# Performance work log

Hardware: AMD Instinct MI355X
Metric: run time of the kernel (lower is better)

## Reference

```python
import jax, jax.numpy as jnp
import numpy as np
import math

B, S, H, E, TOPK, NHEADS = 8, 512, 1024, 8, 2, 8
CAP = int(B * S * 1.5 * TOPK / E)  # 1536


def _linear(x, w, b):
    # torch nn.Linear convention: y = x @ w.T + b, w: [out, in]
    return x @ w.T + b


def _mha(x, in_w, in_b, out_w, out_b, n_heads):
    # torch nn.MultiheadAttention self-attention, eval mode (no dropout)
    Bx, Sx, D = x.shape
    dh = D // n_heads
    qkv = x @ in_w.T + in_b                      # [B,S,3D]
    q, k, v = jnp.split(qkv, 3, axis=-1)
    def heads(t):
        return t.reshape(Bx, Sx, n_heads, dh).transpose(0, 2, 1, 3)  # [B,h,S,dh]
    q, k, v = heads(q), heads(k), heads(v)
    scores = jnp.einsum('bhqd,bhkd->bhqk', q, k) / math.sqrt(dh)
    attn = jax.nn.softmax(scores, axis=-1)
    o = jnp.einsum('bhqk,bhkd->bhqd', attn, v)   # [B,h,S,dh]
    o = o.transpose(0, 2, 1, 3).reshape(Bx, Sx, D)
    return o @ out_w.T + out_b


def setup_inputs() -> dict:
    key = jax.random.key(0)
    ks = jax.random.split(key, 24)
    sc = 0.02
    d = {
        'hidden_states': jax.random.normal(ks[0], (B, S, H), jnp.float32),
        'pos_emb': jax.random.normal(ks[1], (S, H), jnp.float32) * sc,
        'se_w1': jax.random.normal(ks[2], (H // 4, 1), jnp.float32) * sc,
        'se_b1': jnp.zeros((H // 4,), jnp.float32),
        'se_w2': jax.random.normal(ks[3], (H // 4, H // 4), jnp.float32) * sc,
        'se_b2': jnp.zeros((H // 4,), jnp.float32),
        'sexp_w': jax.random.normal(ks[4], (H, H // 4), jnp.float32) * sc,
        'sexp_b': jnp.zeros((H,), jnp.float32),
        'te_w1': jax.random.normal(ks[5], (H, H + 2), jnp.float32) * sc,
        'te_b1': jnp.zeros((H,), jnp.float32),
        'te_w2': jax.random.normal(ks[6], (H, H), jnp.float32) * sc,
        'te_b2': jnp.zeros((H,), jnp.float32),
        'attn_in_w': jax.random.normal(ks[7], (3 * H, H), jnp.float32) * sc,
        'attn_in_b': jnp.zeros((3 * H,), jnp.float32),
        'attn_out_w': jax.random.normal(ks[8], (H, H), jnp.float32) * sc,
        'attn_out_b': jnp.zeros((H,), jnp.float32),
        'tr_w1': jax.random.normal(ks[9], (H, H), jnp.float32) * sc,
        'tr_b1': jnp.zeros((H,), jnp.float32),
        'tr_w2': jax.random.normal(ks[10], (E, H), jnp.float32) * sc,
        'tr_b2': jnp.zeros((E,), jnp.float32),
    }
    return d


def reference(hidden_states, pos_emb, se_w1, se_b1, se_w2, se_b2, sexp_w, sexp_b,
              te_w1, te_b1, te_w2, te_b2, attn_in_w, attn_in_b, attn_out_w, attn_out_b,
              tr_w1, tr_b1, tr_w2, tr_b2):
    b, s, h = hidden_states.shape
    timestamps = jnp.arange(s, dtype=hidden_states.dtype)           # [S]
    seasonality = jnp.sin(timestamps * 2 * jnp.pi / 24)             # [S]
    ts_b = jnp.broadcast_to(timestamps, (b, s))
    se_b = jnp.broadcast_to(seasonality, (b, s))

    position_embeddings = pos_emb[:s][None]                          # [1,S,H]
    seas = jax.nn.relu(_linear(se_b[..., None], se_w1, se_b1))       # [B,S,H/4]
    seas = _linear(seas, se_w2, se_b2)
    seasonal_embeddings = _linear(seas, sexp_w, sexp_b)              # [B,S,H]

    time_features = jnp.stack([ts_b, se_b], axis=-1)                 # [B,S,2]
    combined = jnp.concatenate([hidden_states, time_features], -1)   # [B,S,H+2]
    enc = jax.nn.relu(_linear(combined, te_w1, te_b1))
    enc = _linear(enc, te_w2, te_b2)
    enc = enc + position_embeddings + seasonal_embeddings
    enc = _mha(enc, attn_in_w, attn_in_b, attn_out_w, attn_out_b, NHEADS)

    logits = _linear(jax.nn.relu(_linear(enc, tr_w1, tr_b1)), tr_w2, tr_b2)  # [B,S,E]
    router_probs = jax.nn.softmax(logits, axis=-1)
    top_k_probs, top_k_idx = jax.lax.top_k(router_probs, TOPK)
    top_k_probs = top_k_probs / top_k_probs.sum(-1, keepdims=True)

    capacity = int(b * s * 1.5 * TOPK / E)
    # top-k indices are distinct per token, so summed one-hots replicate the
    # python loop's slot-0 writes exactly.
    onehot = jax.nn.one_hot(top_k_idx, E, dtype=router_probs.dtype)  # [B,S,K,E]
    disp0 = onehot.sum(axis=2)                                        # [B,S,E]
    comb0 = jnp.einsum('bske,bsk->bse', onehot, top_k_probs)          # [B,S,E]
    dispatch = jnp.zeros((b, s, E, capacity), router_probs.dtype).at[:, :, :, 0].set(disp0)
    combine = jnp.zeros((b, s, E, capacity), router_probs.dtype).at[:, :, :, 0].set(comb0)

    p_mean = router_probs.mean(axis=(0, 1))
    aux_loss = jnp.sum(p_mean * jnp.log(p_mean * E + 1e-9))
    return dispatch, combine, router_probs, aux_loss
```

## Files before the change

### kernel.cpp

```cpp
#include <hip/hip_runtime.h>
#include <hip/hip_bf16.h>


#define Hh 1024

typedef __attribute__((ext_vector_type(8))) short short8v;
typedef __attribute__((ext_vector_type(4))) float f32x4;

static __device__ __forceinline__ ushort f2bf(float x) {
  uint u = __float_as_uint(x);
  u += 0x7FFF + ((u >> 16) & 1);
  return (ushort)(u >> 16);
}
static __device__ __forceinline__ float bf2f(ushort h) {
  return __uint_as_float(((uint)h) << 16);
}

template<int EPI, bool RELU, bool HAS_BN, bool HAS_BSN>
__global__ __launch_bounds__(256, 2) void mgemm_k(
    const ushort* __restrict__ A, int lda, long long sAmaj, long long sAmin, int aHi, int aLo,
    const ushort* __restrict__ Bf, int BNT, int BKC, long long sBmaj, long long sBmin,
    float* __restrict__ Cf, ushort* __restrict__ Ch, int ldc, long long sCmaj, long long sCmin,
    int splitOff,
    ushort* __restrict__ pK, ushort* __restrict__ pV,
    int Kd, int zdiv,
    const float* __restrict__ bN, const float* __restrict__ bSN, int ldbs, int smod,
    float alpha)
{
  int gx = gridDim.x, gy = gridDim.y;
  int lin = (blockIdx.z * gy + blockIdx.y) * gx + blockIdx.x;
  int nwg = gx * gy * gridDim.z;
  int cpx = nwg >> 3;
  int swz = (lin & 7) * cpx + (lin >> 3);
  int bz = swz / (gx * gy);
  int rem = swz - bz * (gx * gy);
  int by = rem / gx, bx = rem - by * gx;

  int zj = bz / zdiv, zi = bz - zj * zdiv;
  A += (size_t)zj * sAmaj + (size_t)zi * sAmin;
  const ushort* bfb = Bf + (size_t)zj * sBmaj + (size_t)zi * sBmin;
  long long coff = (long long)zj * sCmaj + (long long)zi * sCmin;

  int m0 = by * 128, n0 = bx * 128;

  __shared__ __align__(16) ushort smem[16384];

  int t = threadIdx.x;
  int l = t & 63, w = t >> 6;
  int wm = w >> 1, wn = w & 1;

  f32x4 acc[4][4];
#pragma unroll
  for (int i = 0; i < 4; ++i)
#pragma unroll
    for (int j = 0; j < 4; ++j) acc[i][j] = (f32x4){0.f, 0.f, 0.f, 0.f};

  int srow = t >> 1;
  int sc = (t & 1) * 2;
  const ushort* gAh = A + (size_t)(m0 + srow) * lda + aHi + sc * 8;
  const ushort* gAl = A + (size_t)(m0 + srow) * lda + aLo + sc * 8;
  int wsw = ((srow >> 1) & 7) << 4;
  int wo0 = (srow * 64 + sc * 16) ^ wsw;
  int wo1 = wo0 ^ 16;

  int aoff[4];
#pragma unroll
  for (int mi = 0; mi < 4; ++mi) {
    int row = wm * 64 + mi * 16 + (l & 15);
    aoff[mi] = (row * 64 + (l >> 4) * 16) ^ (((row >> 1) & 7) << 4);
  }

  const ushort* bph[4];
  const ushort* bpl[4];
  int ntg0 = (n0 >> 4) + wn * 4;
#pragma unroll
  for (int ni = 0; ni < 4; ++ni) {
    bph[ni] = bfb + ((size_t)(ntg0 + ni) * BKC) * 512 + l * 8;
    bpl[ni] = bfb + ((size_t)(BNT + ntg0 + ni) * BKC) * 512 + l * 8;
  }

  int4 a0h0, a0h1, a0l0, a0l1, a1h0, a1h1, a1l0, a1l1;
  short8v B0h[4], B0l[4], B1h[4], B1l[4];

#define LOADA0(s) { a0h0 = *(const int4*)(gAh + (s)*32); a0h1 = *(const int4*)(gAh + (s)*32 + 8); \
                    a0l0 = *(const int4*)(gAl + (s)*32); a0l1 = *(const int4*)(gAl + (s)*32 + 8); }
#define LOADA1(s) { a1h0 = *(const int4*)(gAh + (s)*32); a1h1 = *(const int4*)(gAh + (s)*32 + 8); \
                    a1l0 = *(const int4*)(gAl + (s)*32); a1l1 = *(const int4*)(gAl + (s)*32 + 8); }
#define STOREA(h0, h1, l0, l1, base) { char* nb = (char*)smem + (base); \
    *(int4*)(nb + wo0) = h0; *(int4*)(nb + wo1) = h1; \
    *(int4*)(nb + 8192 + wo0) = l0; *(int4*)(nb + 8192 + wo1) = l1; }
#define LOADB(BH, BL, s) { _Pragma("unroll") \
    for (int ni = 0; ni < 4; ++ni) { \
      BH[ni] = *(const short8v*)(bph[ni] + (size_t)(s) * 512); \
      BL[ni] = *(const short8v*)(bpl[ni] + (size_t)(s) * 512); } }
#define MFMA_STEP(ahb, alb, BH, BL) { \
    short8v ah[4], al[4]; \
    _Pragma("unroll") for (int mi = 0; mi < 4; ++mi) \
      ah[mi] = *(const short8v*)((char*)smem + (ahb) + aoff[mi]); \
    _Pragma("unroll") for (int mi = 0; mi < 4; ++mi) \
      al[mi] = *(const short8v*)((char*)smem + (alb) + aoff[mi]); \
    _Pragma("unroll") for (int ni = 0; ni < 4; ++ni) \
      _Pragma("unroll") for (int mi = 0; mi < 4; ++mi) \
        acc[mi][ni] = __builtin_amdgcn_mfma_f32_16x16x32_bf16(ah[mi], BH[ni], acc[mi][ni], 0, 0, 0); \
    _Pragma("unroll") for (int ni = 0; ni < 4; ++ni) \
      _Pragma("unroll") for (int mi = 0; mi < 4; ++mi) \
        acc[mi][ni] = __builtin_amdgcn_mfma_f32_16x16x32_bf16(al[mi], BH[ni], acc[mi][ni], 0, 0, 0); \
    _Pragma("unroll") for (int ni = 0; ni < 4; ++ni) \
      _Pragma("unroll") for (int mi = 0; mi < 4; ++mi) \
        acc[mi][ni] = __builtin_amdgcn_mfma_f32_16x16x32_bf16(ah[mi], BL[ni], acc[mi][ni], 0, 0, 0); }

  int nt = Kd >> 5;
  LOADA0(0); LOADB(B0h, B0l, 0);
  LOADA1(1); LOADB(B1h, B1l, 1);
  STOREA(a0h0, a0h1, a0l0, a0l1, 0);
  __syncthreads();
  for (int s2 = 0; s2 < nt; s2 += 2) {
    if (s2 + 2 < nt) LOADA0(s2 + 2);
    MFMA_STEP(0, 8192, B0h, B0l);
    if (s2 + 2 < nt) LOADB(B0h, B0l, s2 + 2);
    STOREA(a1h0, a1h1, a1l0, a1l1, 16384);
    __syncthreads();
    if (s2 + 3 < nt) LOADA1(s2 + 3);
    MFMA_STEP(16384, 24576, B1h, B1l);
    if (s2 + 3 < nt) LOADB(B1h, B1l, s2 + 3);
    if (s2 + 2 < nt) STOREA(a0h0, a0h1, a0l0, a0l1, 0);
    __syncthreads();
  }
#undef LOADA0
#undef LOADA1
#undef STOREA
#undef LOADB
#undef MFMA_STEP

#pragma unroll
  for (int mi = 0; mi < 4; ++mi)
#pragma unroll
    for (int j = 0; j < 4; ++j) {
      int m = m0 + wm * 64 + mi * 16 + (l >> 4) * 4 + j;
#pragma unroll
      for (int ni = 0; ni < 4; ++ni) {
        int n = n0 + wn * 64 + ni * 16 + (l & 15);
        float x = acc[mi][ni][j] * alpha;
        if (HAS_BN) x += bN[n];
        if (HAS_BSN) x += bSN[(size_t)(m % smod) * ldbs + n];
        if (RELU) x = fmaxf(x, 0.f);
        acc[mi][ni][j] = x;
      }
    }

  if (EPI == 0) {
    float* Fs = (float*)smem;
#pragma unroll
    for (int p = 0; p < 2; ++p) {
      __syncthreads();
      if (wm == p) {
#pragma unroll
        for (int mi = 0; mi < 4; ++mi)
#pragma unroll
          for (int j = 0; j < 4; ++j) {
            int r = mi * 16 + (l >> 4) * 4 + j;
#pragma unroll
            for (int ni = 0; ni < 4; ++ni) {
              int c = wn * 64 + ni * 16 + (l & 15);
              *(float*)((char*)Fs + ((r * 512 + c * 4) ^ ((r & 7) << 4))) = acc[mi][ni][j];
            }
          }
      }
      __syncthreads();
#pragma unroll
      for (int r8 = 0; r8 < 8; ++r8) {
        int idx = r8 * 256 + t;
        int row = idx >> 5, slot = idx & 31;
        int4 v = *(const int4*)((char*)Fs + ((row * 512 + slot * 16) ^ ((row & 7) << 4)));
        *(int4*)(Cf + coff + (size_t)(m0 + p * 64 + row) * ldc + n0 + slot * 4) = v;
      }
    }
  } else {
    __syncthreads();
    ushort* Es = smem;
    bool isQ = (EPI == 1) || (n0 < 1024);
    bool isK = (EPI == 2) && !isQ && (n0 < 2048);
    int bb = m0 >> 9, s0 = m0 & 511;
    int hh2 = isK ? ((n0 - 1024) >> 7) : ((n0 - 2048) >> 7);
    size_t kvb = (size_t)(bb * 8 + hh2) * 131072;
#pragma unroll
    for (int pass = 0; pass < 2; ++pass) {
      if (isQ) {
#pragma unroll
        for (int mi = 0; mi < 4; ++mi)
#pragma unroll
          for (int j = 0; j < 4; ++j) {
            int lr = wm * 64 + mi * 16 + (l >> 4) * 4 + j;
#pragma unroll
            for (int ni = 0; ni < 4; ++ni) {
              int lcb = (wn * 64 + ni * 16 + (l & 15)) * 2;
              float x = acc[mi][ni][j];
              ushort h = f2bf(x);
              ushort vv = (pass == 0) ? h : f2bf(x - bf2f(h));
              *(ushort*)((char*)Es + ((lr * 256 + lcb) ^ ((lr & 7) << 4))) = vv;
            }
          }
      } else if (isK) {
#pragma unroll
        for (int mi = 0; mi < 4; ++mi)
#pragma unroll
          for (int j = 0; j < 4; ++j) {
            int lr = wm * 64 + mi * 16 + (l >> 4) * 4 + j;
#pragma unroll
            for (int ni = 0; ni < 4; ++ni) {
              int lcb = (wn * 64 + ni * 16 + (l & 15)) * 2;
              float x = acc[mi][ni][j];
              ushort h = f2bf(x);
              ushort vv = (pass == 0) ? h : f2bf(x - bf2f(h));
              *(ushort*)((char*)Es + ((lr * 256 + lcb) ^ ((lr & 7) << 4))) = vv;
            }
          }
      } else {
#pragma unroll
        for (int mi = 0; mi < 4; ++mi)
#pragma unroll
          for (int j = 0; j < 4; ++j) {
            int cc = (wm * 64 + mi * 16 + (l >> 4) * 4 + j) * 2;
#pragma unroll
            for (int ni = 0; ni < 4; ++ni) {
              int rr = wn * 64 + ni * 16 + (l & 15);
              float x = acc[mi][ni][j];
              ushort h = f2bf(x);
              ushort vv = (pass == 0) ? h : f2bf(x - bf2f(h));
              *(ushort*)((char*)Es + ((rr * 256 + cc) ^ ((rr & 7) << 4))) = vv;
            }
          }
      }
      __syncthreads();
      if (isQ) {
        int off = (pass == 0) ? 0 : splitOff;
#pragma unroll
        for (int r = 0; r < 8; ++r) {
          int idx = r * 256 + t;
          int row = idx >> 4, cb = (idx & 15) * 16;
          int4 v = *(const int4*)((char*)Es + ((row * 256 + cb) ^ ((row & 7) << 4)));
          *(int4*)((char*)(Ch + coff + (size_t)(m0 + row) * ldc + off + n0) + cb) = v;
        }
      } else if (isK) {
#pragma unroll
        for (int sw = 0; sw < 8; ++sw) {
          int idx = sw * 256 + t;
          int f = idx >> 6, l2 = idx & 63;
          int st = f >> 2, dc = f & 3;
          int row = st * 16 + (l2 & 15);
          int colB = (dc * 32 + ((l2 >> 4) << 3)) * 2;
          short8v v = *(const short8v*)((char*)Es + ((row * 256 + colB) ^ ((row & 7) << 4)));
          *(short8v*)(pK + kvb + (size_t)((pass * 32 + (s0 >> 4) + st) * 4 + dc) * 512 + l2 * 8) = v;
        }
      } else {
#pragma unroll
        for (int sw = 0; sw < 8; ++sw) {
          int idx = sw * 256 + t;
          int f = idx >> 6, l2 = idx & 63;
          int dt = f >> 2, sch = f & 3;
          int row = dt * 16 + (l2 & 15);
          int colB = (sch * 32 + ((l2 >> 4) << 3)) * 2;
          short8v v = *(const short8v*)((char*)Es + ((row * 256 + colB) ^ ((row & 7) << 4)));
          *(short8v*)(pV + kvb + (size_t)((pass * 8 + dt) * 16 + (s0 >> 5) + sch) * 512 + l2 * 8) = v;
        }
      }
      if (pass == 0) __syncthreads();
    }
  }
}

__global__ __launch_bounds__(64) void convertf_k(
    const float* __restrict__ W, int ldw, ushort* __restrict__ Wf, int NT, int KC)
{
  int kc = blockIdx.x, nt2 = blockIdx.y, l = threadIdx.x;
  const float* src = W + (size_t)(nt2 * 16 + (l & 15)) * ldw + kc * 32 + ((l >> 4) << 3);
  ushort h8[8], l8[8];
#pragma unroll
  for (int j = 0; j < 8; ++j) {
    float x = src[j];
    h8[j] = f2bf(x);
    l8[j] = f2bf(x - bf2f(h8[j]));
  }
  *(int4*)(Wf + ((size_t)nt2 * KC + kc) * 512 + l * 8) = *(int4*)h8;
  *(int4*)(Wf + ((size_t)(NT + nt2) * KC + kc) * 512 + l * 8) = *(int4*)l8;
}

__global__ __launch_bounds__(256) void convert_k(
    const float* __restrict__ W, int lda, ushort* __restrict__ Whl, int K)
{
  int r = blockIdx.x;
  int c = threadIdx.x * 4;
  const float* src = W + (size_t)r * lda + c;
  float x0 = src[0], x1 = src[1], x2 = src[2], x3 = src[3];
  ushort4 h, lo;
  h.x = f2bf(x0); lo.x = f2bf(x0 - bf2f(h.x));
  h.y = f2bf(x1); lo.y = f2bf(x1 - bf2f(h.y));
  h.z = f2bf(x2); lo.z = f2bf(x2 - bf2f(h.z));
  h.w = f2bf(x3); lo.w = f2bf(x3 - bf2f(h.w));
  ushort* dst = Whl + (size_t)r * 2 * K;
  *(ushort4*)&dst[c] = h;
  *(ushort4*)&dst[K + c] = lo;
}

__global__ __launch_bounds__(256) void precompute_k(
    const float* __restrict__ pos_emb,
    const float* __restrict__ se_w1, const float* __restrict__ se_b1,
    const float* __restrict__ se_w2, const float* __restrict__ se_b2,
    const float* __restrict__ sexp_w, const float* __restrict__ sexp_b,
    const float* __restrict__ te_w1, const float* __restrict__ te_b1,
    float* __restrict__ psea, float* __restrict__ bias1)
{
  int s = blockIdx.x, t = threadIdx.x;
  float ts = (float)s;
  float se = sinf(((ts * 2.0f) * 3.14159274101257324f) / 24.0f);
  __shared__ float l1[256], l2[256];
  l1[t] = fmaxf(se * se_w1[t] + se_b1[t], 0.f);
  __syncthreads();
  {
    float a = se_b2[t];
    const float* wr = se_w2 + (size_t)t * 256;
    for (int i = 0; i < 256; ++i) a += l1[i] * wr[i];
    l2[t] = a;
  }
  __syncthreads();
#pragma unroll
  for (int r = 0; r < 4; ++r) {
    int h = r * 256 + t;
    float v = sexp_b[h];
    const float* wr = sexp_w + (size_t)h * 256;
    for (int j = 0; j < 256; ++j) v += l2[j] * wr[j];
    psea[s * Hh + h] = pos_emb[s * Hh + h] + v;
    bias1[s * Hh + h] = te_b1[h] + ts * te_w1[(size_t)h * 1026 + 1024]
                                 + se * te_w1[(size_t)h * 1026 + 1025];
  }
}

__global__ __launch_bounds__(256) void softmax2_k(float* __restrict__ S)
{
  int row = blockIdx.x * 4 + (threadIdx.x >> 6);
  int lane = threadIdx.x & 63;
  float* p = S + (size_t)row * 512;
  float4 a = *(float4*)&p[lane * 4];
  float4 b = *(float4*)&p[256 + lane * 4];
  float m = fmaxf(fmaxf(fmaxf(a.x, a.y), fmaxf(a.z, a.w)),
                  fmaxf(fmaxf(b.x, b.y), fmaxf(b.z, b.w)));
#pragma unroll
  for (int off = 32; off; off >>= 1) m = fmaxf(m, __shfl_xor(m, off));
  a.x = expf(a.x - m); a.y = expf(a.y - m); a.z = expf(a.z - m); a.w = expf(a.w - m);
  b.x = expf(b.x - m); b.y = expf(b.y - m); b.z = expf(b.z - m); b.w = expf(b.w - m);
  float s = a.x + a.y + a.z + a.w + b.x + b.y + b.z + b.w;
#pragma unroll
  for (int off = 32; off; off >>= 1) s += __shfl_xor(s, off);
  float inv = 1.f / s;
  a.x *= inv; a.y *= inv; a.z *= inv; a.w *= inv;
  b.x *= inv; b.y *= inv; b.z *= inv; b.w *= inv;
  ushort* u = (ushort*)S + (size_t)row * 1024;
  ushort4 ha, la, hb, lb;
  ha.x = f2bf(a.x); la.x = f2bf(a.x - bf2f(ha.x));
  ha.y = f2bf(a.y); la.y = f2bf(a.y - bf2f(ha.y));
  ha.z = f2bf(a.z); la.z = f2bf(a.z - bf2f(ha.z));
  ha.w = f2bf(a.w); la.w = f2bf(a.w - bf2f(ha.w));
  hb.x = f2bf(b.x); lb.x = f2bf(b.x - bf2f(hb.x));
  hb.y = f2bf(b.y); lb.y = f2bf(b.y - bf2f(hb.y));
  hb.z = f2bf(b.z); lb.z = f2bf(b.z - bf2f(hb.z));
  hb.w = f2bf(b.w); lb.w = f2bf(b.w - bf2f(hb.w));
  *(ushort4*)&u[lane * 4] = ha;
  *(ushort4*)&u[512 + lane * 4] = la;
  *(ushort4*)&u[256 + lane * 4] = hb;
  *(ushort4*)&u[768 + lane * 4] = lb;
}

__global__ __launch_bounds__(256) void tr2_k(
    const float* __restrict__ h1, const float* __restrict__ w,
    const float* __restrict__ bias, float* __restrict__ logits)
{
  int wid = threadIdx.x >> 6, lane = threadIdx.x & 63;
  int t = blockIdx.x * 4 + wid;
  const float* x = h1 + (size_t)t * Hh;
  float acc[8];
#pragma unroll
  for (int e = 0; e < 8; ++e) acc[e] = 0.f;
  for (int k = lane; k < Hh; k += 64) {
    float xv = x[k];
#pragma unroll
    for (int e = 0; e < 8; ++e) acc[e] += xv * w[e * Hh + k];
  }
#pragma unroll
  for (int e = 0; e < 8; ++e) {
#pragma unroll
    for (int off = 32; off; off >>= 1) acc[e] += __shfl_xor(acc[e], off);
  }
  if (lane == 0) {
#pragma unroll
    for (int e = 0; e < 8; ++e) logits[(size_t)t * 8 + e] = acc[e] + bias[e];
  }
}

__global__ __launch_bounds__(256) void fill0_k(float4* __restrict__ p, long long n4)
{
  long long i = (long long)blockIdx.x * 256 + threadIdx.x;
  long long stride = (long long)gridDim.x * 256;
  float4 z = make_float4(0.f, 0.f, 0.f, 0.f);
  for (; i < n4; i += stride) p[i] = z;
}

__global__ __launch_bounds__(256) void router_k(
    float* __restrict__ out, float* __restrict__ partials)
{
  int t = blockIdx.x * 256 + threadIdx.x;
  float* lg = out + 100663296 + (size_t)t * 8;
  float p[8];
#pragma unroll
  for (int e = 0; e < 8; ++e) p[e] = lg[e];
  float m = p[0];
#pragma unroll
  for (int e = 1; e < 8; ++e) m = fmaxf(m, p[e]);
  float s = 0.f;
#pragma unroll
  for (int e = 0; e < 8; ++e) { p[e] = expf(p[e] - m); s += p[e]; }
  float inv = 1.f / s;
#pragma unroll
  for (int e = 0; e < 8; ++e) p[e] *= inv;
#pragma unroll
  for (int e = 0; e < 8; ++e) lg[e] = p[e];

  int i0 = 0; float v0 = p[0];
#pragma unroll
  for (int e = 1; e < 8; ++e) if (p[e] > v0) { v0 = p[e]; i0 = e; }
  int i1 = -1; float v1 = -1.f;
#pragma unroll
  for (int e = 0; e < 8; ++e) if (e != i0 && p[e] > v1) { v1 = p[e]; i1 = e; }
  float wn = 1.f / (v0 + v1);
  size_t db = (size_t)t * (8 * 1536);
  out[db + (size_t)i0 * 1536] = 1.f;
  out[db + (size_t)i1 * 1536] = 1.f;
  out[50331648 + db + (size_t)i0 * 1536] = v0 * wn;
  out[50331648 + db + (size_t)i1 * 1536] = v1 * wn;

  __shared__ float red[256];
#pragma unroll
  for (int e = 0; e < 8; ++e) {
    red[threadIdx.x] = p[e];
    __syncthreads();
    for (int st = 128; st; st >>= 1) {
      if (threadIdx.x < st) red[threadIdx.x] += red[threadIdx.x + st];
      __syncthreads();
    }
    if (threadIdx.x == 0) partials[blockIdx.x * 8 + e] = red[0];
    __syncthreads();
  }
}

__global__ __launch_bounds__(64) void aux_k(float* __restrict__ partials,
                                            float* __restrict__ out)
{
  int lane = threadIdx.x;
  float v = 0.f;
  if (lane < 8) {
    float s = 0.f;
    for (int b = 0; b < 16; ++b) s += partials[b * 8 + lane];
    float pm = s / 4096.f;
    v = pm * logf(pm * 8.f + 1e-9f);
  }
#pragma unroll
  for (int off = 4; off; off >>= 1) v += __shfl_xor(v, off);
  if (lane == 0) out[100696064] = v;
  partials[lane] = 0.f;
  partials[64 + lane] = 0.f;
}

extern "C" void kernel_launch(void* const* d_in, const int* in_sizes, int n_in,
                              void* d_out, int out_size, void* d_ws, size_t ws_size,
                              hipStream_t stream)
{
  const float* hidden = (const float*)d_in[0];
  const float* pos_emb = (const float*)d_in[1];
  const float* se_w1 = (const float*)d_in[2];
  const float* se_b1 = (const float*)d_in[3];
  const float* se_w2 = (const float*)d_in[4];
  const float* se_b2 = (const float*)d_in[5];
  const float* sexp_w = (const float*)d_in[6];
  const float* sexp_b = (const float*)d_in[7];
  const float* te_w1 = (const float*)d_in[8];
  const float* te_b1 = (const float*)d_in[9];
  const float* te_w2 = (const float*)d_in[10];
  const float* te_b2 = (const float*)d_in[11];
  const float* ain_w = (const float*)d_in[12];
  const float* ain_b = (const float*)d_in[13];
  const float* aout_w = (const float*)d_in[14];
  const float* aout_b = (const float*)d_in[15];
  const float* tr_w1 = (const float*)d_in[16];
  const float* tr_b1 = (const float*)d_in[17];
  const float* tr_w2 = (const float*)d_in[18];
  const float* tr_b2 = (const float*)d_in[19];
  float* out = (float*)d_out;

  char* arena = (char*)d_out;
  ushort* W1f  = (ushort*)(arena + 0);
  ushort* W2f  = (ushort*)(arena + 4194304);
  ushort* Waf  = (ushort*)(arena + 8388608);
  ushort* Wof  = (ushort*)(arena + 20971520);
  ushort* Wtf  = (ushort*)(arena + 25165824);
  ushort* hid2 = (ushort*)(arena + 29360128);
  ushort* enc1 = (ushort*)(arena + 46137344);
  ushort* enc2 = (ushort*)(arena + 62914560);
  ushort* qbuf = (ushort*)(arena + 79691776);
  ushort* Kf   = (ushort*)(arena + 96468992);
  ushort* Vf   = (ushort*)(arena + 113246208);
  float*  scor = (float*)(arena + 130023424);
  ushort* attno= (ushort*)(arena + 197132288);
  ushort* encf = (ushort*)(arena + 213909504);
  float*  h1   = (float*)(arena + 230686720);
  float*  psea = (float*)(arena + 247463936);
  float*  bias1= (float*)(arena + 249561088);
  float*  parts= out + 51380224;
  float*  lgts = out + 100663296;

  convertf_k<<<dim3(32, 64), 64, 0, stream>>>(te_w1, 1026, W1f, 64, 32);
  convertf_k<<<dim3(32, 64), 64, 0, stream>>>(te_w2, 1024, W2f, 64, 32);
  convertf_k<<<dim3(32, 192), 64, 0, stream>>>(ain_w, 1024, Waf, 192, 32);
  convertf_k<<<dim3(32, 64), 64, 0, stream>>>(aout_w, 1024, Wof, 64, 32);
  convertf_k<<<dim3(32, 64), 64, 0, stream>>>(tr_w1, 1024, Wtf, 64, 32);
  convert_k<<<4096, 256, 0, stream>>>(hidden, 1024, hid2, 1024);

  precompute_k<<<512, 256, 0, stream>>>(pos_emb, se_w1, se_b1, se_w2, se_b2,
                                        sexp_w, sexp_b, te_w1, te_b1, psea, bias1);

  mgemm_k<1, true, false, true><<<dim3(8, 32, 1), 256, 0, stream>>>(
      hid2, 2048, 0, 0, 0, 1024,
      W1f, 64, 32, 0, 0,
      nullptr, enc1, 2048, 0, 0, 1024, nullptr, nullptr,
      1024, 1, nullptr, bias1, 1024, 512, 1.f);

  mgemm_k<1, false, true, true><<<dim3(8, 32, 1), 256, 0, stream>>>(
      enc1, 2048, 0, 0, 0, 1024,
      W2f, 64, 32, 0, 0,
      nullptr, enc2, 2048, 0, 0, 1024, nullptr, nullptr,
      1024, 1, te_b2, psea, 1024, 512, 1.f);

  mgemm_k<2, false, true, false><<<dim3(24, 32, 1), 256, 0, stream>>>(
      enc2, 2048, 0, 0, 0, 1024,
      Waf, 192, 32, 0, 0,
      nullptr, qbuf, 2048, 0, 0, 1024, Kf, Vf,
      1024, 1, ain_b, nullptr, 1, 1, 1.f);

  mgemm_k<0, false, false, false><<<dim3(4, 4, 64), 256, 0, stream>>>(
      qbuf, 2048, 1048576, 128, 0, 1024,
      Kf, 32, 4, 1048576, 131072,
      scor, nullptr, 512, 2097152, 262144, 0, nullptr, nullptr,
      128, 8, nullptr, nullptr, 1, 1, 0.08838834764831845f);

  softmax2_k<<<8192, 256, 0, stream>>>(scor);

  mgemm_k<1, false, false, false><<<dim3(1, 4, 64), 256, 0, stream>>>(
      (const ushort*)scor, 1024, 4194304, 524288, 0, 512,
      Vf, 8, 16, 1048576, 131072,
      nullptr, attno, 2048, 1048576, 128, 1024, nullptr, nullptr,
      512, 8, nullptr, nullptr, 1, 1, 1.f);

  mgemm_k<1, false, true, false><<<dim3(8, 32, 1), 256, 0, stream>>>(
      attno, 2048, 0, 0, 0, 1024,
      Wof, 64, 32, 0, 0,
      nullptr, encf, 2048, 0, 0, 1024, nullptr, nullptr,
      1024, 1, aout_b, nullptr, 1, 1, 1.f);

  mgemm_k<0, true, true, false><<<dim3(8, 32, 1), 256, 0, stream>>>(
      encf, 2048, 0, 0, 0, 1024,
      Wtf, 64, 32, 0, 0,
      h1, nullptr, 1024, 0, 0, 0, nullptr, nullptr,
      1024, 1, tr_b1, nullptr, 1, 1, 1.f);

  tr2_k<<<1024, 256, 0, stream>>>(h1, tr_w2, tr_b2, lgts);

  fill0_k<<<4096, 256, 0, stream>>>((float4*)out, 25165824LL);

  router_k<<<16, 256, 0, stream>>>(out, parts);
  aux_k<<<1, 64, 0, stream>>>(parts, out);
}
```

Measured before the change: 481.4 us.

## Fuse QK^T, softmax and PV into a single attention kernel

Replaces the three-kernel attention path (score GEMM writing fp32 scores, a separate softmax pass, and a PV GEMM reading split-bf16 probabilities) with one fused kernel. Each 512-thread block keeps a 128x512 score tile in registers, reduces row max and sum through shared memory, and feeds split-bf16 probabilities through LDS into the PV MFMAs. This removes the large score-buffer round trip through global memory and two launches. The five weight-conversion launches are also merged into one, and the Q/K epilogue branches are deduplicated. The cost is very high register pressure from the 128-float score accumulator per thread plus an extra occupancy constraint.

```diff
diff --git a/kernel.cpp b/kernel.cpp
--- a/kernel.cpp
+++ b/kernel.cpp
@@ -185,22 +185,7 @@
     size_t kvb = (size_t)(bb * 8 + hh2) * 131072;
 #pragma unroll
     for (int pass = 0; pass < 2; ++pass) {
-      if (isQ) {
-#pragma unroll
-        for (int mi = 0; mi < 4; ++mi)
-#pragma unroll
-          for (int j = 0; j < 4; ++j) {
-            int lr = wm * 64 + mi * 16 + (l >> 4) * 4 + j;
-#pragma unroll
-            for (int ni = 0; ni < 4; ++ni) {
-              int lcb = (wn * 64 + ni * 16 + (l & 15)) * 2;
-              float x = acc[mi][ni][j];
-              ushort h = f2bf(x);
-              ushort vv = (pass == 0) ? h : f2bf(x - bf2f(h));
-              *(ushort*)((char*)Es + ((lr * 256 + lcb) ^ ((lr & 7) << 4))) = vv;
-            }
-          }
-      } else if (isK) {
+      if (!(EPI == 2 && !isQ && !isK)) {
 #pragma unroll
         for (int mi = 0; mi < 4; ++mi)
 #pragma unroll
@@ -269,10 +254,265 @@
   }
 }
 
-__global__ __launch_bounds__(64) void convertf_k(
-    const float* __restrict__ W, int ldw, ushort* __restrict__ Wf, int NT, int KC)
-{
-  int kc = blockIdx.x, nt2 = blockIdx.y, l = threadIdx.x;
+__global__ __launch_bounds__(512, 2) void attn_k(
+    const ushort* __restrict__ qbuf, const ushort* __restrict__ Kf,
+    const ushort* __restrict__ Vf, ushort* __restrict__ attno)
+{
+  int qt = blockIdx.x;
+  int bh = blockIdx.y;
+  int b = bh >> 3, h = bh & 7;
+
+  __shared__ __align__(16) ushort smem[32768];
+  __shared__ float rowred[1024];
+
+  int t = threadIdx.x;
+  int l = t & 63, w = t >> 6;
+  int wm = w >> 2, wn = w & 3;
+
+  {
+    int srow = t >> 2, sc = t & 3;
+    const ushort* gQ = qbuf + (size_t)(b * 512 + qt * 128 + srow) * 2048 + h * 128 + sc * 8;
+    int wo = (srow * 64 + sc * 16) ^ (((srow >> 1) & 7) << 4);
+#pragma unroll
+    for (int ks = 0; ks < 4; ++ks) {
+      int4 vh = *(const int4*)(gQ + ks * 32);
+      int4 vl = *(const int4*)(gQ + 1024 + ks * 32);
+      *(int4*)((char*)smem + ks * 8192 + wo) = vh;
+      *(int4*)((char*)smem + 32768 + ks * 8192 + wo) = vl;
+    }
+  }
+
+  int aoff[4];
+#pragma unroll
+  for (int mi = 0; mi < 4; ++mi) {
+    int row = wm * 64 + mi * 16 + (l & 15);
+    aoff[mi] = (row * 64 + (l >> 4) * 16) ^ (((row >> 1) & 7) << 4);
+  }
+
+  __syncthreads();
+
+  f32x4 S[4][4][2];
+#pragma unroll
+  for (int c = 0; c < 4; ++c)
+#pragma unroll
+    for (int mi = 0; mi < 4; ++mi)
+#pragma unroll
+      for (int ni = 0; ni < 2; ++ni) S[c][mi][ni] = (f32x4){0.f, 0.f, 0.f, 0.f};
+
+  const ushort* Kb = Kf + (size_t)bh * 131072 + l * 8;
+#pragma unroll
+  for (int c = 0; c < 4; ++c) {
+#pragma unroll
+    for (int ks = 0; ks < 4; ++ks) {
+      short8v bhf[2], blf[2], ahf[4], alf[4];
+#pragma unroll
+      for (int ni = 0; ni < 2; ++ni) {
+        int ntk = c * 8 + wn * 2 + ni;
+        bhf[ni] = *(const short8v*)(Kb + (size_t)(ntk * 4 + ks) * 512);
+        blf[ni] = *(const short8v*)(Kb + (size_t)((32 + ntk) * 4 + ks) * 512);
+      }
+#pragma unroll
+      for (int mi = 0; mi < 4; ++mi) {
+        ahf[mi] = *(const short8v*)((char*)smem + ks * 8192 + aoff[mi]);
+        alf[mi] = *(const short8v*)((char*)smem + 32768 + ks * 8192 + aoff[mi]);
+      }
+#pragma unroll
+      for (int ni = 0; ni < 2; ++ni)
+#pragma unroll
+        for (int mi = 0; mi < 4; ++mi)
+          S[c][mi][ni] = __builtin_amdgcn_mfma_f32_16x16x32_bf16(ahf[mi], bhf[ni], S[c][mi][ni], 0, 0, 0);
+#pragma unroll
+      for (int ni = 0; ni < 2; ++ni)
+#pragma unroll
+        for (int mi = 0; mi < 4; ++mi)
+          S[c][mi][ni] = __builtin_amdgcn_mfma_f32_16x16x32_bf16(alf[mi], bhf[ni], S[c][mi][ni], 0, 0, 0);
+#pragma unroll
+      for (int ni = 0; ni < 2; ++ni)
+#pragma unroll
+        for (int mi = 0; mi < 4; ++mi)
+          S[c][mi][ni] = __builtin_amdgcn_mfma_f32_16x16x32_bf16(ahf[mi], blf[ni], S[c][mi][ni], 0, 0, 0);
+    }
+  }
+
+  const float scale = 0.08838834764831845f;
+  float inv16[4][4];
+  {
+    float mx[4][4];
+#pragma unroll
+    for (int mi = 0; mi < 4; ++mi)
+#pragma unroll
+      for (int j = 0; j < 4; ++j) {
+        float m2 = -3.0e38f;
+#pragma unroll
+        for (int c = 0; c < 4; ++c)
+#pragma unroll
+          for (int ni = 0; ni < 2; ++ni) m2 = fmaxf(m2, S[c][mi][ni][j]);
+#pragma unroll
+        for (int off = 8; off; off >>= 1) m2 = fmaxf(m2, __shfl_xor(m2, off));
+        mx[mi][j] = m2;
+      }
+    if ((l & 15) == 0) {
+#pragma unroll
+      for (int mi = 0; mi < 4; ++mi)
+#pragma unroll
+        for (int j = 0; j < 4; ++j) {
+          int row = wm * 64 + mi * 16 + (l >> 4) * 4 + j;
+          rowred[wn * 128 + row] = mx[mi][j];
+        }
+    }
+    __syncthreads();
+#pragma unroll
+    for (int mi = 0; mi < 4; ++mi)
+#pragma unroll
+      for (int j = 0; j < 4; ++j) {
+        int row = wm * 64 + mi * 16 + (l >> 4) * 4 + j;
+        float m2 = fmaxf(fmaxf(rowred[row], rowred[128 + row]),
+                         fmaxf(rowred[256 + row], rowred[384 + row]));
+        mx[mi][j] = m2 * scale;
+      }
+    float sm[4][4];
+#pragma unroll
+    for (int mi = 0; mi < 4; ++mi)
+#pragma unroll
+      for (int j = 0; j < 4; ++j) {
+        float s2 = 0.f;
+#pragma unroll
+        for (int c = 0; c < 4; ++c)
+#pragma unroll
+          for (int ni = 0; ni < 2; ++ni) {
+            float p = __expf(fmaf(S[c][mi][ni][j], scale, -mx[mi][j]));
+            S[c][mi][ni][j] = p;
+            s2 += p;
+          }
+#pragma unroll
+        for (int off = 8; off; off >>= 1) s2 += __shfl_xor(s2, off);
+        sm[mi][j] = s2;
+      }
+    if ((l & 15) == 0) {
+#pragma unroll
+      for (int mi = 0; mi < 4; ++mi)
+#pragma unroll
+        for (int j = 0; j < 4; ++j) {
+          int row = wm * 64 + mi * 16 + (l >> 4) * 4 + j;
+          rowred[512 + wn * 128 + row] = sm[mi][j];
+        }
+    }
+    __syncthreads();
+#pragma unroll
+    for (int mi = 0; mi < 4; ++mi)
+#pragma unroll
+      for (int j = 0; j < 4; ++j) {
+        int row = wm * 64 + mi * 16 + (l >> 4) * 4 + j;
+        float s2 = rowred[512 + row] + rowred[640 + row]
+                 + rowred[768 + row] + rowred[896 + row];
+        inv16[mi][j] = 1.f / s2;
+      }
+  }
+
+  f32x4 O[4][2];
+#pragma unroll
+  for (int mi = 0; mi < 4; ++mi)
+#pragma unroll
+    for (int ni = 0; ni < 2; ++ni) O[mi][ni] = (f32x4){0.f, 0.f, 0.f, 0.f};
+
+  const ushort* Vb = Vf + (size_t)bh * 131072 + l * 8;
+#pragma unroll
+  for (int c = 0; c < 4; ++c) {
+    __syncthreads();
+#pragma unroll
+    for (int mi = 0; mi < 4; ++mi)
+#pragma unroll
+      for (int j = 0; j < 4; ++j) {
+        int row = wm * 64 + mi * 16 + (l >> 4) * 4 + j;
+        int sw2 = ((row >> 1) & 7) << 4;
+#pragma unroll
+        for (int ni = 0; ni < 2; ++ni) {
+          float p = S[c][mi][ni][j] * inv16[mi][j];
+          ushort hh = f2bf(p);
+          ushort ll2 = f2bf(p - bf2f(hh));
+          int off = (row * 64 + (ni * 16 + (l & 15)) * 2) ^ sw2;
+          *(ushort*)((char*)smem + wn * 8192 + off) = hh;
+          *(ushort*)((char*)smem + 32768 + wn * 8192 + off) = ll2;
+        }
+      }
+    __syncthreads();
+#pragma unroll
+    for (int ks = 0; ks < 4; ++ks) {
+      short8v pah[4], pal[4], vbh[2], vbl[2];
+#pragma unroll
+      for (int ni = 0; ni < 2; ++ni) {
+        int ntd = wn * 2 + ni;
+        vbh[ni] = *(const short8v*)(Vb + (size_t)(ntd * 16 + c * 4 + ks) * 512);
+        vbl[ni] = *(const short8v*)(Vb + (size_t)((8 + ntd) * 16 + c * 4 + ks) * 512);
+      }
+#pragma unroll
+      for (int mi = 0; mi < 4; ++mi) {
+        pah[mi] = *(const short8v*)((char*)smem + ks * 8192 + aoff[mi]);
+        pal[mi] = *(const short8v*)((char*)smem + 32768 + ks * 8192 + aoff[mi]);
+      }
+#pragma unroll
+      for (int ni = 0; ni < 2; ++ni)
+#pragma unroll
+        for (int mi = 0; mi < 4; ++mi)
+          O[mi][ni] = __builtin_amdgcn_mfma_f32_16x16x32_bf16(pah[mi], vbh[ni], O[mi][ni], 0, 0, 0);
+#pragma unroll
+      for (int ni = 0; ni < 2; ++ni)
+#pragma unroll
+        for (int mi = 0; mi < 4; ++mi)
+          O[mi][ni] = __builtin_amdgcn_mfma_f32_16x16x32_bf16(pal[mi], vbh[ni], O[mi][ni], 0, 0, 0);
+#pragma unroll
+      for (int ni = 0; ni < 2; ++ni)
+#pragma unroll
+        for (int mi = 0; mi < 4; ++mi)
+          O[mi][ni] = __builtin_amdgcn_mfma_f32_16x16x32_bf16(pah[mi], vbl[ni], O[mi][ni], 0, 0, 0);
+    }
+  }
+
+  __syncthreads();
+  ushort* Es = smem;
+  size_t coff = (size_t)b * 1048576 + (size_t)h * 128;
+  int m0 = qt * 128;
+#pragma unroll
+  for (int pass = 0; pass < 2; ++pass) {
+#pragma unroll
+    for (int mi = 0; mi < 4; ++mi)
+#pragma unroll
+      for (int j = 0; j < 4; ++j) {
+        int lr = wm * 64 + mi * 16 + (l >> 4) * 4 + j;
+#pragma unroll
+        for (int ni = 0; ni < 2; ++ni) {
+          int lcb = (wn * 32 + ni * 16 + (l & 15)) * 2;
+          float x = O[mi][ni][j];
+          ushort hh = f2bf(x);
+          ushort vv = (pass == 0) ? hh : f2bf(x - bf2f(hh));
+          *(ushort*)((char*)Es + ((lr * 256 + lcb) ^ ((lr & 7) << 4))) = vv;
+        }
+      }
+    __syncthreads();
+    int off = (pass == 0) ? 0 : 1024;
+#pragma unroll
+    for (int r = 0; r < 4; ++r) {
+      int idx = r * 512 + t;
+      int row = idx >> 4, cb = (idx & 15) * 16;
+      int4 v = *(const int4*)((char*)Es + ((row * 256 + cb) ^ ((row & 7) << 4)));
+      *(int4*)((char*)(attno + coff + (size_t)(m0 + row) * 2048 + off) + cb) = v;
+    }
+    if (pass == 0) __syncthreads();
+  }
+}
+
+__global__ __launch_bounds__(64) void convall_k(
+    const float* __restrict__ te_w1, const float* __restrict__ te_w2,
+    const float* __restrict__ ain_w, const float* __restrict__ aout_w,
+    const float* __restrict__ tr_w1, ushort* __restrict__ base)
+{
+  int kc = blockIdx.x, y = blockIdx.y, l = threadIdx.x;
+  const float* W; int ldw, NT, nt2; ushort* dst;
+  if (y < 64)       { W = te_w1;  ldw = 1026; NT = 64;  nt2 = y;       dst = base; }
+  else if (y < 128) { W = te_w2;  ldw = 1024; NT = 64;  nt2 = y - 64;  dst = base + 2097152; }
+  else if (y < 320) { W = ain_w;  ldw = 1024; NT = 192; nt2 = y - 128; dst = base + 4194304; }
+  else if (y < 384) { W = aout_w; ldw = 1024; NT = 64;  nt2 = y - 320; dst = base + 10485760; }
+  else              { W = tr_w1;  ldw = 1024; NT = 64;  nt2 = y - 384; dst = base + 12582912; }
   const float* src = W + (size_t)(nt2 * 16 + (l & 15)) * ldw + kc * 32 + ((l >> 4) << 3);
   ushort h8[8], l8[8];
 #pragma unroll
@@ -281,8 +521,8 @@
     h8[j] = f2bf(x);
     l8[j] = f2bf(x - bf2f(h8[j]));
   }
-  *(int4*)(Wf + ((size_t)nt2 * KC + kc) * 512 + l * 8) = *(int4*)h8;
-  *(int4*)(Wf + ((size_t)(NT + nt2) * KC + kc) * 512 + l * 8) = *(int4*)l8;
+  *(int4*)(dst + ((size_t)nt2 * 32 + kc) * 512 + l * 8) = *(int4*)h8;
+  *(int4*)(dst + ((size_t)(NT + nt2) * 32 + kc) * 512 + l * 8) = *(int4*)l8;
 }
 
 __global__ __launch_bounds__(256) void convert_k(
@@ -333,41 +573,6 @@
     bias1[s * Hh + h] = te_b1[h] + ts * te_w1[(size_t)h * 1026 + 1024]
                                  + se * te_w1[(size_t)h * 1026 + 1025];
   }
-}
-
-__global__ __launch_bounds__(256) void softmax2_k(float* __restrict__ S)
-{
-  int row = blockIdx.x * 4 + (threadIdx.x >> 6);
-  int lane = threadIdx.x & 63;
-  float* p = S + (size_t)row * 512;
-  float4 a = *(float4*)&p[lane * 4];
-  float4 b = *(float4*)&p[256 + lane * 4];
-  float m = fmaxf(fmaxf(fmaxf(a.x, a.y), fmaxf(a.z, a.w)),
-                  fmaxf(fmaxf(b.x, b.y), fmaxf(b.z, b.w)));
-#pragma unroll
-  for (int off = 32; off; off >>= 1) m = fmaxf(m, __shfl_xor(m, off));
-  a.x = expf(a.x - m); a.y = expf(a.y - m); a.z = expf(a.z - m); a.w = expf(a.w - m);
-  b.x = expf(b.x - m); b.y = expf(b.y - m); b.z = expf(b.z - m); b.w = expf(b.w - m);
-  float s = a.x + a.y + a.z + a.w + b.x + b.y + b.z + b.w;
-#pragma unroll
-  for (int off = 32; off; off >>= 1) s += __shfl_xor(s, off);
-  float inv = 1.f / s;
-  a.x *= inv; a.y *= inv; a.z *= inv; a.w *= inv;
-  b.x *= inv; b.y *= inv; b.z *= inv; b.w *= inv;
-  ushort* u = (ushort*)S + (size_t)row * 1024;
-  ushort4 ha, la, hb, lb;
-  ha.x = f2bf(a.x); la.x = f2bf(a.x - bf2f(ha.x));
-  ha.y = f2bf(a.y); la.y = f2bf(a.y - bf2f(ha.y));
-  ha.z = f2bf(a.z); la.z = f2bf(a.z - bf2f(ha.z));
-  ha.w = f2bf(a.w); la.w = f2bf(a.w - bf2f(ha.w));
-  hb.x = f2bf(b.x); lb.x = f2bf(b.x - bf2f(hb.x));
-  hb.y = f2bf(b.y); lb.y = f2bf(b.y - bf2f(hb.y));
-  hb.z = f2bf(b.z); lb.z = f2bf(b.z - bf2f(hb.z));
-  hb.w = f2bf(b.w); lb.w = f2bf(b.w - bf2f(hb.w));
-  *(ushort4*)&u[lane * 4] = ha;
-  *(ushort4*)&u[512 + lane * 4] = la;
-  *(ushort4*)&u[256 + lane * 4] = hb;
-  *(ushort4*)&u[768 + lane * 4] = lb;
 }
 
 __global__ __launch_bounds__(256) void tr2_k(
@@ -496,18 +701,13 @@
   float* out = (float*)d_out;
 
   char* arena = (char*)d_out;
-  ushort* W1f  = (ushort*)(arena + 0);
-  ushort* W2f  = (ushort*)(arena + 4194304);
-  ushort* Waf  = (ushort*)(arena + 8388608);
-  ushort* Wof  = (ushort*)(arena + 20971520);
-  ushort* Wtf  = (ushort*)(arena + 25165824);
+  ushort* Wbase= (ushort*)(arena + 0);
   ushort* hid2 = (ushort*)(arena + 29360128);
   ushort* enc1 = (ushort*)(arena + 46137344);
   ushort* enc2 = (ushort*)(arena + 62914560);
   ushort* qbuf = (ushort*)(arena + 79691776);
   ushort* Kf   = (ushort*)(arena + 96468992);
   ushort* Vf   = (ushort*)(arena + 113246208);
-  float*  scor = (float*)(arena + 130023424);
   ushort* attno= (ushort*)(arena + 197132288);
   ushort* encf = (ushort*)(arena + 213909504);
   float*  h1   = (float*)(arena + 230686720);
@@ -516,57 +716,40 @@
   float*  parts= out + 51380224;
   float*  lgts = out + 100663296;
 
-  convertf_k<<<dim3(32, 64), 64, 0, stream>>>(te_w1, 1026, W1f, 64, 32);
-  convertf_k<<<dim3(32, 64), 64, 0, stream>>>(te_w2, 1024, W2f, 64, 32);
-  convertf_k<<<dim3(32, 192), 64, 0, stream>>>(ain_w, 1024, Waf, 192, 32);
-  convertf_k<<<dim3(32, 64), 64, 0, stream>>>(aout_w, 1024, Wof, 64, 32);
-  convertf_k<<<dim3(32, 64), 64, 0, stream>>>(tr_w1, 1024, Wtf, 64, 32);
+  convall_k<<<dim3(32, 448), 64, 0, stream>>>(te_w1, te_w2, ain_w, aout_w, tr_w1, Wbase);
   convert_k<<<4096, 256, 0, stream>>>(hidden, 1024, hid2, 1024);
-
   precompute_k<<<512, 256, 0, stream>>>(pos_emb, se_w1, se_b1, se_w2, se_b2,
                                         sexp_w, sexp_b, te_w1, te_b1, psea, bias1);
 
   mgemm_k<1, true, false, true><<<dim3(8, 32, 1), 256, 0, stream>>>(
       hid2, 2048, 0, 0, 0, 1024,
-      W1f, 64, 32, 0, 0,
+      Wbase, 64, 32, 0, 0,
       nullptr, enc1, 2048, 0, 0, 1024, nullptr, nullptr,
       1024, 1, nullptr, bias1, 1024, 512, 1.f);
 
   mgemm_k<1, false, true, true><<<dim3(8, 32, 1), 256, 0, stream>>>(
       enc1, 2048, 0, 0, 0, 1024,
-      W2f, 64, 32, 0, 0,
+      Wbase + 2097152, 64, 32, 0, 0,
       nullptr, enc2, 2048, 0, 0, 1024, nullptr, nullptr,
       1024, 1, te_b2, psea, 1024, 512, 1.f);
 
   mgemm_k<2, false, true, false><<<dim3(24, 32, 1), 256, 0, stream>>>(
       enc2, 2048, 0, 0, 0, 1024,
-      Waf, 192, 32, 0, 0,
+      Wbase + 4194304, 192, 32, 0, 0,
       nullptr, qbuf, 2048, 0, 0, 1024, Kf, Vf,
       1024, 1, ain_b, nullptr, 1, 1, 1.f);
 
-  mgemm_k<0, false, false, false><<<dim3(4, 4, 64), 256, 0, stream>>>(
-      qbuf, 2048, 1048576, 128, 0, 1024,
-      Kf, 32, 4, 1048576, 131072,
-      scor, nullptr, 512, 2097152, 262144, 0, nullptr, nullptr,
-      128, 8, nullptr, nullptr, 1, 1, 0.08838834764831845f);
-
-  softmax2_k<<<8192, 256, 0, stream>>>(scor);
-
-  mgemm_k<1, false, false, false><<<dim3(1, 4, 64), 256, 0, stream>>>(
-      (const ushort*)scor, 1024, 4194304, 524288, 0, 512,
-      Vf, 8, 16, 1048576, 131072,
-      nullptr, attno, 2048, 1048576, 128, 1024, nullptr, nullptr,
-      512, 8, nullptr, nullptr, 1, 1, 1.f);
+  attn_k<<<dim3(4, 64), 512, 0, stream>>>(qbuf, Kf, Vf, attno);
 
   mgemm_k<1, false, true, false><<<dim3(8, 32, 1), 256, 0, stream>>>(
       attno, 2048, 0, 0, 0, 1024,
-      Wof, 64, 32, 0, 0,
+      Wbase + 10485760, 64, 32, 0, 0,
       nullptr, encf, 2048, 0, 0, 1024, nullptr, nullptr,
       1024, 1, aout_b, nullptr, 1, 1, 1.f);
 
   mgemm_k<0, true, true, false><<<dim3(8, 32, 1), 256, 0, stream>>>(
       encf, 2048, 0, 0, 0, 1024,
-      Wtf, 64, 32, 0, 0,
+      Wbase + 12582912, 64, 32, 0, 0,
       h1, nullptr, 1024, 0, 0, 0, nullptr, nullptr,
       1024, 1, tr_b1, nullptr, 1, 1, 1.f);
 
```

New measurement: 460.4 us, median of 2. -4.4%, faster.
